# Kernel tuning notes

Measured on AMD Instinct MI355X. Metric: run time of the kernel, lower is better.

The kernel has to match this reference:

```python
import jax, jax.numpy as jnp
import numpy as np

ROUTINGS = 3


def setup_inputs() -> dict:
    key = jax.random.key(0)
    k1, k2 = jax.random.split(key)
    B, I, D_in = 64, 512, 128   # batch, input_num_capsule, input_dim_capsule
    N, O = 32, 64               # num_capsule, dim_capsule
    x = jax.random.normal(k1, (B, I, D_in), dtype=jnp.float32)
    # he_normal-ish init for W [N, I, O, D_in]
    W = jax.random.normal(k2, (N, I, O, D_in), dtype=jnp.float32) * np.float32(np.sqrt(2.0 / D_in))
    return {"x": x, "W": W}


def reference(x, W):
    # inputs_hat[b,n,i,o] = sum_d x[b,i,d] * W[n,i,o,d]
    u = jnp.einsum('bid,niod->bnio', x, W)  # [B, N, I, O]
    b = jnp.zeros(u.shape[:3], dtype=u.dtype)  # [B, N, I]
    outputs = None
    for r in range(ROUTINGS):
        c = jax.nn.softmax(b, axis=1)                    # softmax over num_capsule axis
        outputs = jnp.einsum('bni,bnio->bno', c, u)      # [B, N, O]
        if r < ROUTINGS - 1:
            b = jnp.einsum('bno,bnio->bni', outputs, u)  # agreement update
    # faithful to source: returns capsule lengths, shape [B, N]
    return jnp.sqrt(jnp.sum(jnp.square(outputs), axis=2))
```

## Files before the change

### kernel.cpp

```cpp
#include <hip/hip_runtime.h>

typedef unsigned short ushort_t;
typedef _Float16 half_t;
typedef __attribute__((ext_vector_type(8))) unsigned short ushort8;
typedef __attribute__((ext_vector_type(8))) _Float16 half8;
typedef __attribute__((ext_vector_type(8))) short bf16x8;
typedef __attribute__((ext_vector_type(4))) float f32x4;

#define BB 64
#define II 512
#define DD 128
#define NN 32
#define OO 64

__device__ inline ushort_t f2bf(float f) {
  unsigned int u = __float_as_uint(f);
  u += 0x7FFF + ((u >> 16) & 1);
  return (ushort_t)(u >> 16);
}
__device__ inline float bf2f(ushort_t h) {
  return __uint_as_float(((unsigned int)h) << 16);
}

__device__ inline void load8u(const half_t* p, float* a) {
  half8 v = *(const half8*)p;
  #pragma unroll
  for (int e = 0; e < 8; ++e) a[e] = (float)v[e];
}

__global__ __launch_bounds__(256) void k_compute_u(
    const float* __restrict__ x, const float* __restrict__ W,
    half_t* __restrict__ u)
{
  __shared__ ushort_t Ah[64*128] __attribute__((aligned(16)));
  __shared__ ushort_t Al[64*128] __attribute__((aligned(16)));
  __shared__ ushort_t Bh[64*128] __attribute__((aligned(16)));
  __shared__ ushort_t Bl[64*128] __attribute__((aligned(16)));
  __shared__ float    Cs[64*64]  __attribute__((aligned(16)));
  const int tid  = threadIdx.x;
  const int i    = blockIdx.x;
  const int n0   = blockIdx.y * 8;
  const int w    = tid >> 6;
  const int lane = tid & 63;

  for (int k = 0; k < 4; ++k) {
    int flat = tid + 256*k;
    int row  = flat >> 4;
    int c8   = flat & 15;
    const float* gp = x + ((size_t)row*II + i)*DD + c8*8;
    float4 f0 = *(const float4*)(gp);
    float4 f1 = *(const float4*)(gp + 4);
    float fv[8] = {f0.x,f0.y,f0.z,f0.w,f1.x,f1.y,f1.z,f1.w};
    ushort8 h, l;
    #pragma unroll
    for (int e = 0; e < 8; ++e) {
      ushort_t hh = f2bf(fv[e]); h[e] = hh; l[e] = f2bf(fv[e] - bf2f(hh));
    }
    int off = (row*256 + c8*16) ^ ((row & 7) << 4);
    *(ushort8*)((char*)Ah + off) = h;
    *(ushort8*)((char*)Al + off) = l;
  }

  for (int j = 0; j < 8; ++j) {
    int n = n0 + j;
    __syncthreads();

    const float* wbase = W + (((size_t)n*II + i)*OO)*DD;
    for (int k = 0; k < 4; ++k) {
      int flat = tid + 256*k;
      int row  = flat >> 4;
      int c8   = flat & 15;
      const float* gp = wbase + row*DD + c8*8;
      float4 f0 = *(const float4*)(gp);
      float4 f1 = *(const float4*)(gp + 4);
      float fv[8] = {f0.x,f0.y,f0.z,f0.w,f1.x,f1.y,f1.z,f1.w};
      ushort8 h, l;
      #pragma unroll
      for (int e = 0; e < 8; ++e) {
        ushort_t hh = f2bf(fv[e]); h[e] = hh; l[e] = f2bf(fv[e] - bf2f(hh));
      }
      int off = (row*256 + c8*16) ^ ((row & 7) << 4);
      *(ushort8*)((char*)Bh + off) = h;
      *(ushort8*)((char*)Bl + off) = l;
    }
    __syncthreads();

    f32x4 zero = {0.f, 0.f, 0.f, 0.f};
    f32x4 acc[4];
    #pragma unroll
    for (int ot = 0; ot < 4; ++ot) acc[ot] = zero;

    #pragma unroll
    for (int kk = 0; kk < 4; ++kk) {
      int ra   = w*16 + (lane & 15);
      int aoff = (ra*256 + kk*64 + ((lane >> 4) << 4)) ^ ((ra & 7) << 4);
      bf16x8 ah = *(bf16x8*)((char*)Ah + aoff);
      bf16x8 al = *(bf16x8*)((char*)Al + aoff);
      #pragma unroll
      for (int ot = 0; ot < 4; ++ot) {
        int rb   = ot*16 + (lane & 15);
        int boff = (rb*256 + kk*64 + ((lane >> 4) << 4)) ^ ((rb & 7) << 4);
        bf16x8 bh = *(bf16x8*)((char*)Bh + boff);
        bf16x8 bl = *(bf16x8*)((char*)Bl + boff);
        acc[ot] = __builtin_amdgcn_mfma_f32_16x16x32_bf16(ah, bh, acc[ot], 0, 0, 0);
        acc[ot] = __builtin_amdgcn_mfma_f32_16x16x32_bf16(al, bh, acc[ot], 0, 0, 0);
        acc[ot] = __builtin_amdgcn_mfma_f32_16x16x32_bf16(ah, bl, acc[ot], 0, 0, 0);
      }
    }

    #pragma unroll
    for (int ot = 0; ot < 4; ++ot)
      #pragma unroll
      for (int r = 0; r < 4; ++r) {
        int row = w*16 + ((lane >> 4) << 2) + r;
        int col = ot*16 + (lane & 15);
        Cs[row*64 + col] = acc[ot][r];
      }
    __syncthreads();

    for (int k = 0; k < 2; ++k) {
      int flat = tid + 256*k;
      int row  = flat >> 3;
      int c8   = flat & 7;
      const float* sp = Cs + row*64 + c8*8;
      half8 v;
      #pragma unroll
      for (int e = 0; e < 8; ++e) v[e] = (half_t)sp[e];
      *(half8*)(u + (((size_t)row*NN + n)*II + i)*OO + c8*8) = v;
    }
  }
}

__global__ __launch_bounds__(256) void k_round0(
    const half_t* __restrict__ u, float* __restrict__ out0)
{
  __shared__ float sPart[32*65];
  const int tid = threadIdx.x;
  const int bn  = blockIdx.x;
  const int ip  = tid >> 3;
  const int o8  = tid & 7;
  const half_t* base = u + (size_t)bn * (II*OO);
  float a[8];
  #pragma unroll
  for (int e = 0; e < 8; ++e) a[e] = 0.f;
  for (int i = ip; i < II; i += 32) {
    float t[8];
    load8u(base + (size_t)i*OO + o8*8, t);
    #pragma unroll
    for (int e = 0; e < 8; ++e) a[e] += t[e];
  }
  #pragma unroll
  for (int e = 0; e < 8; ++e) sPart[ip*65 + o8*8 + e] = a[e];
  for (int step = 16; step >= 1; step >>= 1) {
    __syncthreads();
    if (ip < step) {
      #pragma unroll
      for (int e = 0; e < 8; ++e)
        sPart[ip*65 + o8*8 + e] += sPart[(ip+step)*65 + o8*8 + e];
    }
  }
  __syncthreads();
  if (tid < 64) out0[(size_t)bn*OO + tid] = sPart[tid] * (1.f/32.f);
}

__global__ __launch_bounds__(256, 2) void k_round_reg(
    const half_t* __restrict__ u, const float* __restrict__ out_prev,
    float* __restrict__ part)
{
  __shared__ float sOut[NN*OO];
  __shared__ float sP[NN][16][9];
  __shared__ float sLog[16][NN+1];
  __shared__ float sC[16][NN+1];
  const int tid = threadIdx.x;
  const int ic  = blockIdx.x;
  const int b   = blockIdx.y;
  const int n   = tid >> 3;
  const int q   = tid & 7;

  for (int k = 0; k < 8; ++k) {
    int flat = tid + 256*k;
    sOut[flat] = out_prev[(size_t)b*NN*OO + flat];
  }
  float a8[8];
  #pragma unroll
  for (int e = 0; e < 8; ++e) a8[e] = 0.f;
  __syncthreads();

  const half_t* ubase = u + ((size_t)b*NN + n)*II*OO;
  for (int s = 0; s < 4; ++s) {
    const int i0 = ic*64 + s*16;
    float r[16][8];
    #pragma unroll
    for (int ii = 0; ii < 16; ++ii) {
      load8u(ubase + (size_t)(i0+ii)*OO + q*8, r[ii]);
      float acc = 0.f;
      #pragma unroll
      for (int e = 0; e < 8; ++e) acc += r[ii][e] * sOut[n*OO + q*8 + e];
      sP[n][ii][q] = acc;
    }
    __syncthreads();
    #pragma unroll
    for (int h = 0; h < 2; ++h) {
      int ii = q + h*8;
      float sum = 0.f;
      #pragma unroll
      for (int q2 = 0; q2 < 8; ++q2) sum += sP[n][ii][q2];
      sLog[ii][n] = sum;
    }
    __syncthreads();
    #pragma unroll
    for (int h = 0; h < 2; ++h) {
      int ii = q + h*8;
      float m = -1e30f;
      #pragma unroll
      for (int n2 = 0; n2 < NN; ++n2) m = fmaxf(m, sLog[ii][n2]);
      float ss = 0.f;
      #pragma unroll
      for (int n2 = 0; n2 < NN; ++n2) ss += __expf(sLog[ii][n2] - m);
      sC[ii][n] = __expf(sLog[ii][n] - m) / ss;
    }
    __syncthreads();
    #pragma unroll
    for (int ii = 0; ii < 16; ++ii) {
      float cv = sC[ii][n];
      #pragma unroll
      for (int e = 0; e < 8; ++e) a8[e] += cv * r[ii][e];
    }
  }
  float* dst = part + (((size_t)ic*BB + b)*NN + n)*OO + q*8;
  #pragma unroll
  for (int e = 0; e < 8; ++e) dst[e] = a8[e];
}

__global__ __launch_bounds__(256) void k_reduce_part(
    const float* __restrict__ part, float* __restrict__ out_next)
{
  const int j = blockIdx.x*256 + threadIdx.x;
  const size_t O = (size_t)BB*NN*OO;
  float s = 0.f;
  #pragma unroll
  for (int k = 0; k < 8; ++k) s += part[(size_t)k*O + j];
  out_next[j] = s;
}

__global__ __launch_bounds__(256) void k_len(
    const float* __restrict__ out2, float* __restrict__ dout)
{
  int t = blockIdx.x*blockDim.x + threadIdx.x;
  if (t < BB*NN) {
    const float* p = out2 + (size_t)t*OO;
    float s = 0.f;
    #pragma unroll
    for (int o = 0; o < OO; ++o) { float f = p[o]; s += f*f; }
    dout[t] = sqrtf(s);
  }
}

extern "C" void kernel_launch(void* const* d_in, const int* in_sizes, int n_in,
                              void* d_out, int out_size, void* d_ws, size_t ws_size,
                              hipStream_t stream)
{
  const float* x = (const float*)d_in[0];
  const float* W = (const float*)d_in[1];
  float* dout = (float*)d_out;

  const size_t U = (size_t)BB*NN*II*OO;
  const size_t O = (size_t)BB*NN*OO;

  half_t* u   = (half_t*)d_ws;
  float* out0 = (float*)((char*)d_ws + U*2);
  float* out1 = out0 + O;
  float* out2 = out1 + O;
  float* part = out2 + O;

  k_compute_u  <<<dim3(II, 4),  dim3(256), 0, stream>>>(x, W, u);
  k_round0     <<<dim3(BB*NN),  dim3(256), 0, stream>>>(u, out0);
  k_round_reg  <<<dim3(8, BB),  dim3(256), 0, stream>>>(u, out0, part);
  k_reduce_part<<<dim3(512),    dim3(256), 0, stream>>>(part, out1);
  k_round_reg  <<<dim3(8, BB),  dim3(256), 0, stream>>>(u, out1, part);
  k_reduce_part<<<dim3(512),    dim3(256), 0, stream>>>(part, out2);
  hipLaunchKernelGGL(k_len, dim3(8), dim3(256), 0, stream, out2, dout);
}
```

Baseline: 218.0 us.

## Fuse routing round zero into u computation via per-chunk partial sums

The first routing round (uniform softmax, so a plain sum over input capsules) is folded into the u-computation kernel. Each block now covers 8 input capsules and 4 output capsules and accumulates the GEMM results in registers, writing per-chunk partials that a new reduction kernel sums. This removes a full re-read of the fp16 u tensor in the old round-0 kernel. In exchange the grid drops from 2048 to 512 blocks, the kernel holds 64 extra accumulator floats per thread under a 2-waves launch bound, and x is re-staged once per i per block.

```diff
diff --git a/kernel.cpp b/kernel.cpp
--- a/kernel.cpp
+++ b/kernel.cpp
@@ -28,9 +28,9 @@
   for (int e = 0; e < 8; ++e) a[e] = (float)v[e];
 }
 
-__global__ __launch_bounds__(256) void k_compute_u(
+__global__ __launch_bounds__(256, 2) void k_compute_u_r0(
     const float* __restrict__ x, const float* __restrict__ W,
-    half_t* __restrict__ u)
+    half_t* __restrict__ u, float* __restrict__ part0)
 {
   __shared__ ushort_t Ah[64*128] __attribute__((aligned(16)));
   __shared__ ushort_t Al[64*128] __attribute__((aligned(16)));
@@ -38,39 +38,25 @@
   __shared__ ushort_t Bl[64*128] __attribute__((aligned(16)));
   __shared__ float    Cs[64*64]  __attribute__((aligned(16)));
   const int tid  = threadIdx.x;
-  const int i    = blockIdx.x;
-  const int n0   = blockIdx.y * 8;
+  const int ic   = blockIdx.x;
+  const int nj   = blockIdx.y;
   const int w    = tid >> 6;
   const int lane = tid & 63;
 
-  for (int k = 0; k < 4; ++k) {
-    int flat = tid + 256*k;
-    int row  = flat >> 4;
-    int c8   = flat & 15;
-    const float* gp = x + ((size_t)row*II + i)*DD + c8*8;
-    float4 f0 = *(const float4*)(gp);
-    float4 f1 = *(const float4*)(gp + 4);
-    float fv[8] = {f0.x,f0.y,f0.z,f0.w,f1.x,f1.y,f1.z,f1.w};
-    ushort8 h, l;
-    #pragma unroll
-    for (int e = 0; e < 8; ++e) {
-      ushort_t hh = f2bf(fv[e]); h[e] = hh; l[e] = f2bf(fv[e] - bf2f(hh));
-    }
-    int off = (row*256 + c8*16) ^ ((row & 7) << 4);
-    *(ushort8*)((char*)Ah + off) = h;
-    *(ushort8*)((char*)Al + off) = l;
-  }
-
-  for (int j = 0; j < 8; ++j) {
-    int n = n0 + j;
-    __syncthreads();
-
-    const float* wbase = W + (((size_t)n*II + i)*OO)*DD;
+  f32x4 acc0[4][4];
+  #pragma unroll
+  for (int j = 0; j < 4; ++j)
+    #pragma unroll
+    for (int ot = 0; ot < 4; ++ot) acc0[j][ot] = {0.f, 0.f, 0.f, 0.f};
+
+  #pragma unroll 1
+  for (int it = 0; it < 8; ++it) {
+    const int i = ic*8 + it;
     for (int k = 0; k < 4; ++k) {
       int flat = tid + 256*k;
       int row  = flat >> 4;
       int c8   = flat & 15;
-      const float* gp = wbase + row*DD + c8*8;
+      const float* gp = x + ((size_t)row*II + i)*DD + c8*8;
       float4 f0 = *(const float4*)(gp);
       float4 f1 = *(const float4*)(gp + 4);
       float fv[8] = {f0.x,f0.y,f0.z,f0.w,f1.x,f1.y,f1.z,f1.w};
@@ -80,87 +66,115 @@
         ushort_t hh = f2bf(fv[e]); h[e] = hh; l[e] = f2bf(fv[e] - bf2f(hh));
       }
       int off = (row*256 + c8*16) ^ ((row & 7) << 4);
-      *(ushort8*)((char*)Bh + off) = h;
-      *(ushort8*)((char*)Bl + off) = l;
-    }
-    __syncthreads();
-
-    f32x4 zero = {0.f, 0.f, 0.f, 0.f};
-    f32x4 acc[4];
-    #pragma unroll
-    for (int ot = 0; ot < 4; ++ot) acc[ot] = zero;
-
-    #pragma unroll
-    for (int kk = 0; kk < 4; ++kk) {
-      int ra   = w*16 + (lane & 15);
-      int aoff = (ra*256 + kk*64 + ((lane >> 4) << 4)) ^ ((ra & 7) << 4);
-      bf16x8 ah = *(bf16x8*)((char*)Ah + aoff);
-      bf16x8 al = *(bf16x8*)((char*)Al + aoff);
+      *(ushort8*)((char*)Ah + off) = h;
+      *(ushort8*)((char*)Al + off) = l;
+    }
+
+    #pragma unroll
+    for (int j = 0; j < 4; ++j) {
+      const int n = nj*4 + j;
+      const float* wbase = W + (((size_t)n*II + i)*OO)*DD;
+      for (int k = 0; k < 4; ++k) {
+        int flat = tid + 256*k;
+        int row  = flat >> 4;
+        int c8   = flat & 15;
+        const float* gp = wbase + row*DD + c8*8;
+        float4 f0 = *(const float4*)(gp);
+        float4 f1 = *(const float4*)(gp + 4);
+        float fv[8] = {f0.x,f0.y,f0.z,f0.w,f1.x,f1.y,f1.z,f1.w};
+        ushort8 h, l;
+        #pragma unroll
+        for (int e = 0; e < 8; ++e) {
+          ushort_t hh = f2bf(fv[e]); h[e] = hh; l[e] = f2bf(fv[e] - bf2f(hh));
+        }
+        int off = (row*256 + c8*16) ^ ((row & 7) << 4);
+        *(ushort8*)((char*)Bh + off) = h;
+        *(ushort8*)((char*)Bl + off) = l;
+      }
+      __syncthreads();
+
+      f32x4 zero = {0.f, 0.f, 0.f, 0.f};
+      f32x4 acc[4];
+      #pragma unroll
+      for (int ot = 0; ot < 4; ++ot) acc[ot] = zero;
+
+      #pragma unroll
+      for (int kk = 0; kk < 4; ++kk) {
+        int ra   = w*16 + (lane & 15);
+        int aoff = (ra*256 + kk*64 + ((lane >> 4) << 4)) ^ ((ra & 7) << 4);
+        bf16x8 ah = *(bf16x8*)((char*)Ah + aoff);
+        bf16x8 al = *(bf16x8*)((char*)Al + aoff);
+        #pragma unroll
+        for (int ot = 0; ot < 4; ++ot) {
+          int rb   = ot*16 + (lane & 15);
+          int boff = (rb*256 + kk*64 + ((lane >> 4) << 4)) ^ ((rb & 7) << 4);
+          bf16x8 bh = *(bf16x8*)((char*)Bh + boff);
+          bf16x8 bl = *(bf16x8*)((char*)Bl + boff);
+          acc[ot] = __builtin_amdgcn_mfma_f32_16x16x32_bf16(ah, bh, acc[ot], 0, 0, 0);
+          acc[ot] = __builtin_amdgcn_mfma_f32_16x16x32_bf16(al, bh, acc[ot], 0, 0, 0);
+          acc[ot] = __builtin_amdgcn_mfma_f32_16x16x32_bf16(ah, bl, acc[ot], 0, 0, 0);
+        }
+      }
+
       #pragma unroll
       for (int ot = 0; ot < 4; ++ot) {
-        int rb   = ot*16 + (lane & 15);
-        int boff = (rb*256 + kk*64 + ((lane >> 4) << 4)) ^ ((rb & 7) << 4);
-        bf16x8 bh = *(bf16x8*)((char*)Bh + boff);
-        bf16x8 bl = *(bf16x8*)((char*)Bl + boff);
-        acc[ot] = __builtin_amdgcn_mfma_f32_16x16x32_bf16(ah, bh, acc[ot], 0, 0, 0);
-        acc[ot] = __builtin_amdgcn_mfma_f32_16x16x32_bf16(al, bh, acc[ot], 0, 0, 0);
-        acc[ot] = __builtin_amdgcn_mfma_f32_16x16x32_bf16(ah, bl, acc[ot], 0, 0, 0);
-      }
-    }
-
+        acc0[j][ot] += acc[ot];
+        #pragma unroll
+        for (int r = 0; r < 4; ++r) {
+          int row = w*16 + ((lane >> 4) << 2) + r;
+          int col = ot*16 + (lane & 15);
+          Cs[row*64 + col] = acc[ot][r];
+        }
+      }
+      __syncthreads();
+
+      for (int k = 0; k < 2; ++k) {
+        int flat = tid + 256*k;
+        int row  = flat >> 3;
+        int c8   = flat & 7;
+        const float* sp = Cs + row*64 + c8*8;
+        half8 v;
+        #pragma unroll
+        for (int e = 0; e < 8; ++e) v[e] = (half_t)sp[e];
+        *(half8*)(u + (((size_t)row*NN + n)*II + i)*OO + c8*8) = v;
+      }
+    }
+  }
+
+  #pragma unroll
+  for (int j = 0; j < 4; ++j) {
+    const int n = nj*4 + j;
+    __syncthreads();
     #pragma unroll
     for (int ot = 0; ot < 4; ++ot)
       #pragma unroll
       for (int r = 0; r < 4; ++r) {
         int row = w*16 + ((lane >> 4) << 2) + r;
         int col = ot*16 + (lane & 15);
-        Cs[row*64 + col] = acc[ot][r];
-      }
-    __syncthreads();
-
+        Cs[row*64 + col] = acc0[j][ot][r];
+      }
+    __syncthreads();
     for (int k = 0; k < 2; ++k) {
       int flat = tid + 256*k;
       int row  = flat >> 3;
       int c8   = flat & 7;
       const float* sp = Cs + row*64 + c8*8;
-      half8 v;
-      #pragma unroll
-      for (int e = 0; e < 8; ++e) v[e] = (half_t)sp[e];
-      *(half8*)(u + (((size_t)row*NN + n)*II + i)*OO + c8*8) = v;
-    }
-  }
-}
-
-__global__ __launch_bounds__(256) void k_round0(
-    const half_t* __restrict__ u, float* __restrict__ out0)
-{
-  __shared__ float sPart[32*65];
-  const int tid = threadIdx.x;
-  const int bn  = blockIdx.x;
-  const int ip  = tid >> 3;
-  const int o8  = tid & 7;
-  const half_t* base = u + (size_t)bn * (II*OO);
-  float a[8];
-  #pragma unroll
-  for (int e = 0; e < 8; ++e) a[e] = 0.f;
-  for (int i = ip; i < II; i += 32) {
-    float t[8];
-    load8u(base + (size_t)i*OO + o8*8, t);
-    #pragma unroll
-    for (int e = 0; e < 8; ++e) a[e] += t[e];
-  }
-  #pragma unroll
-  for (int e = 0; e < 8; ++e) sPart[ip*65 + o8*8 + e] = a[e];
-  for (int step = 16; step >= 1; step >>= 1) {
-    __syncthreads();
-    if (ip < step) {
-      #pragma unroll
-      for (int e = 0; e < 8; ++e)
-        sPart[ip*65 + o8*8 + e] += sPart[(ip+step)*65 + o8*8 + e];
-    }
-  }
-  __syncthreads();
-  if (tid < 64) out0[(size_t)bn*OO + tid] = sPart[tid] * (1.f/32.f);
+      float* dst = part0 + (((size_t)ic*BB + row)*NN + n)*OO + c8*8;
+      *(f32x4*)dst       = *(const f32x4*)sp;
+      *(f32x4*)(dst + 4) = *(const f32x4*)(sp + 4);
+    }
+  }
+}
+
+__global__ __launch_bounds__(256) void k_reduce0(
+    const float* __restrict__ part0, float* __restrict__ out0)
+{
+  const int j = blockIdx.x*256 + threadIdx.x;
+  const size_t O = (size_t)BB*NN*OO;
+  float s = 0.f;
+  #pragma unroll
+  for (int k = 0; k < 64; ++k) s += part0[(size_t)k*O + j];
+  out0[j] = s * (1.f/32.f);
 }
 
 __global__ __launch_bounds__(256, 2) void k_round_reg(
@@ -267,17 +281,18 @@
   const size_t U = (size_t)BB*NN*II*OO;
   const size_t O = (size_t)BB*NN*OO;
 
-  half_t* u   = (half_t*)d_ws;
-  float* out0 = (float*)((char*)d_ws + U*2);
-  float* out1 = out0 + O;
-  float* out2 = out1 + O;
-  float* part = out2 + O;
-
-  k_compute_u  <<<dim3(II, 4),  dim3(256), 0, stream>>>(x, W, u);
-  k_round0     <<<dim3(BB*NN),  dim3(256), 0, stream>>>(u, out0);
-  k_round_reg  <<<dim3(8, BB),  dim3(256), 0, stream>>>(u, out0, part);
-  k_reduce_part<<<dim3(512),    dim3(256), 0, stream>>>(part, out1);
-  k_round_reg  <<<dim3(8, BB),  dim3(256), 0, stream>>>(u, out1, part);
-  k_reduce_part<<<dim3(512),    dim3(256), 0, stream>>>(part, out2);
+  half_t* u    = (half_t*)d_ws;
+  float* part0 = (float*)((char*)d_ws + U*2);
+  float* out0  = part0 + 64*O;
+  float* out1  = out0 + O;
+  float* out2  = out1 + O;
+  float* part  = out2 + O;
+
+  k_compute_u_r0<<<dim3(64, 8), dim3(256), 0, stream>>>(x, W, u, part0);
+  k_reduce0     <<<dim3(512),   dim3(256), 0, stream>>>(part0, out0);
+  k_round_reg   <<<dim3(8, BB), dim3(256), 0, stream>>>(u, out0, part);
+  k_reduce_part <<<dim3(512),   dim3(256), 0, stream>>>(part, out1);
+  k_round_reg   <<<dim3(8, BB), dim3(256), 0, stream>>>(u, out1, part);
+  k_reduce_part <<<dim3(512),   dim3(256), 0, stream>>>(part, out2);
   hipLaunchKernelGGL(k_len, dim3(8), dim3(256), 0, stream, out2, dout);
 }
```

New measurement: 282.2 us. 1.29x slower.
